# Kernel tuning notes

Hardware: AMD Instinct MI355X
Metric: run time of the kernel (lower is better)

Reference implementation:

```python
import jax, jax.numpy as jnp
import numpy as np
from jax import lax

HID, PROJ, DYN = 256, 256, 64
HW, BS, NQ = 6400, 16, 100


def setup_inputs() -> dict:
    key = jax.random.key(0)
    ks = jax.random.split(key, 10)
    p = lambda k, shape: jax.random.normal(k, shape, jnp.float32) * 0.02
    return {
        "query_feat": jax.random.normal(ks[0], (HW, BS, HID), jnp.float32),
        "support_feat": jax.random.normal(ks[1], (NQ, BS, HID), jnp.float32),
        "h": 80,
        "w": 80,
        "Wq": p(ks[2], (HID, PROJ)), "bq": jnp.zeros((PROJ,), jnp.float32),
        "Ws": p(ks[3], (HID, PROJ)), "bsp": jnp.zeros((PROJ,), jnp.float32),
        "W1": p(ks[4], (PROJ, DYN)), "b1": jnp.zeros((DYN,), jnp.float32),
        "W2": p(ks[5], (DYN, HID)), "b2": jnp.zeros((HID,), jnp.float32),
    }


def reference(query_feat, support_feat, h, w, Wq, bq, Ws, bsp, W1, b1, W2, b2):
    # query_feat: [hw, bs, c] -> [bs, hw, c]; support_feat: [nq, bs, c] -> [bs, nq, c]
    qf = jnp.transpose(query_feat, (1, 0, 2))
    sf = jnp.transpose(support_feat, (1, 0, 2))
    bsz, nq = sf.shape[0], sf.shape[1]
    hw = h * w

    fs_proj = sf @ Ws + bsp                      # [bs, nq, proj]
    fq_proj = qf @ Wq + bq                       # [bs, hw, proj]
    pattern = jnp.tanh(jax.nn.relu(fs_proj @ W1 + b1) @ W2 + b2)
    fs_feat = (pattern + 1.0) * fs_proj          # [bs, nq, proj]

    # bmm(fq, fs^T).T -> [bs, nq, hw]
    sim = jnp.einsum("bkp,bnp->bnk", fq_proj, fs_feat)
    similarity = sim.reshape(bsz, nq, h, w)

    # coordinate grid: x varies along w, y along h; flattened [hw, 2]
    gy = jnp.arange(h, dtype=jnp.float32) + 0.5
    gx = jnp.arange(w, dtype=jnp.float32) + 0.5
    X, Y = jnp.meshgrid(gx, gy, indexing="xy")  # each [h, w]
    coord = jnp.stack([X, Y], axis=-1).reshape(hw, 2)
    side = jnp.array([w, h], dtype=jnp.float32)

    sm = jax.nn.softmax(sim, axis=-1)            # [bs, nq, hw]
    proposal_for_loss = jnp.einsum("bnk,kd->bnd", sm, coord) / side

    # argmax peak -> one-hot -> 3x3 max-pool dilation (note (w,h) reshape per original)
    max_pos = jnp.argmax(sim, axis=-1)           # [bs, nq]
    max_mask = jax.nn.one_hot(max_pos, hw, dtype=jnp.float32).reshape(bsz, nq, w, h)
    local_mask = lax.reduce_window(
        max_mask, -jnp.inf, lax.max,
        window_dimensions=(1, 1, 3, 3), window_strides=(1, 1, 1, 1),
        padding=[(0, 0), (0, 0), (1, 1), (1, 1)],
    ).reshape(bsz, nq, hw)

    local_sm = sm * local_mask
    local_sm = local_sm / (jnp.sum(local_sm, axis=-1, keepdims=True) + 1e-10)
    proposals = jnp.einsum("bnk,kd->bnd", local_sm, coord) / side

    return proposal_for_loss, similarity, proposals
```

## Files before the change

### kernel.cpp

```cpp
#include <hip/hip_runtime.h>

#define HID 256
#define PROJ 256
#define DYN 64
#define HWD 6400
#define BSZ 16
#define NQ 100
#define HH 80
#define WW 80

typedef unsigned short u16;
typedef u16 u16x8 __attribute__((ext_vector_type(8)));
typedef __bf16 bf16x8 __attribute__((ext_vector_type(8)));
typedef float f32x4 __attribute__((ext_vector_type(4)));

__device__ __forceinline__ float bf2f(u16 h) {
    union { unsigned u; float f; } c; c.u = ((unsigned)h) << 16; return c.f;
}
__device__ __forceinline__ u16 f2bf(float f) {
    union { float f; unsigned u; } c; c.f = f;
    return (u16)((c.u + 0x7FFFu + ((c.u >> 16) & 1u)) >> 16);
}

__global__ __launch_bounds__(1024, 1) void kpre(
    const float* __restrict__ support,
    const float* __restrict__ Wq, const float* __restrict__ bq,
    const float* __restrict__ Ws, const float* __restrict__ bsp,
    const float* __restrict__ W1, const float* __restrict__ b1,
    const float* __restrict__ W2, const float* __restrict__ b2,
    u16* __restrict__ pack, float* __restrict__ cvec)
{
    const int c = blockIdx.x;
    const int b = blockIdx.y;
    const int t = threadIdx.x;

    __shared__ __align__(16) float sf_t[HID][8];
    __shared__ __align__(16) float part[4][8][256];
    __shared__ __align__(16) float fsp[8][PROJ];
    __shared__ __align__(16) float hidp[2][8][DYN];
    __shared__ __align__(16) float hid[8][DYN];
    __shared__ __align__(16) float fsf_t[PROJ][8];
    __shared__ float cacc[8][4];

    const int g = t >> 8;
    const int p = t & 255;

    {
        const int nl = t >> 7;
        const int i0 = (t & 127) * 2;
        const int n = c * 8 + nl;
        float v0 = 0.f, v1 = 0.f;
        if (n < NQ) {
            const float* sp = support + (size_t)n * (BSZ * HID) + (size_t)b * HID + i0;
            const float2 a = *reinterpret_cast<const float2*>(sp);
            v0 = a.x; v1 = a.y;
        }
        sf_t[i0][nl] = v0;
        sf_t[i0 + 1][nl] = v1;
    }
    __syncthreads();

    {
        float acc[8];
        #pragma unroll
        for (int n = 0; n < 8; ++n) acc[n] = 0.f;
        const int ibase = g * 64;
        float w[64];
        #pragma unroll
        for (int j = 0; j < 64; ++j)
            w[j] = Ws[(size_t)(ibase + j) * PROJ + p];
        __builtin_amdgcn_sched_barrier(0);
        #pragma unroll
        for (int j = 0; j < 64; ++j) {
            const f32x4 s0 = *reinterpret_cast<const f32x4*>(&sf_t[ibase + j][0]);
            const f32x4 s1 = *reinterpret_cast<const f32x4*>(&sf_t[ibase + j][4]);
            acc[0] += s0[0] * w[j]; acc[1] += s0[1] * w[j];
            acc[2] += s0[2] * w[j]; acc[3] += s0[3] * w[j];
            acc[4] += s1[0] * w[j]; acc[5] += s1[1] * w[j];
            acc[6] += s1[2] * w[j]; acc[7] += s1[3] * w[j];
        }
        #pragma unroll
        for (int n = 0; n < 8; ++n) part[g][n][p] = acc[n];
    }
    __syncthreads();
    {
        const int na = t >> 8;
        const float bb = bsp[p];
        #pragma unroll
        for (int k = 0; k < 2; ++k) {
            const int n = na + k * 4;
            fsp[n][p] = part[0][n][p] + part[1][n][p] + part[2][n][p] + part[3][n][p] + bb;
        }
    }
    __syncthreads();

    {
        const int ph = t >> 9;
        const int n = (t >> 6) & 7;
        const int d = t & 63;
        float a = 0.f;
        const int pb0 = ph * 128;
        #pragma unroll
        for (int pb = 0; pb < 128; pb += 64) {
            float w[64];
            #pragma unroll
            for (int j = 0; j < 64; ++j)
                w[j] = W1[(size_t)(pb0 + pb + j) * DYN + d];
            __builtin_amdgcn_sched_barrier(0);
            #pragma unroll
            for (int j = 0; j < 64; j += 4) {
                const f32x4 s = *reinterpret_cast<const f32x4*>(&fsp[n][pb0 + pb + j]);
                a += s[0] * w[j] + s[1] * w[j + 1] + s[2] * w[j + 2] + s[3] * w[j + 3];
            }
        }
        hidp[ph][n][d] = a;
    }
    __syncthreads();
    if (t < 512) {
        const int n = t >> 6, d = t & 63;
        const float a = hidp[0][n][d] + hidp[1][n][d] + b1[d];
        hid[n][d] = a > 0.f ? a : 0.f;
    }
    __syncthreads();

    {
        const int nh = t >> 8;
        const int n0 = nh * 2, n1 = nh * 2 + 1;
        const float bqv = bq[p];
        const float b2v = b2[p];
        float w[64];
        #pragma unroll
        for (int d = 0; d < 64; ++d) w[d] = W2[(size_t)d * PROJ + p];
        __builtin_amdgcn_sched_barrier(0);
        float a0 = 0.f, a1 = 0.f;
        #pragma unroll
        for (int d0 = 0; d0 < 64; d0 += 4) {
            const f32x4 h0 = *reinterpret_cast<const f32x4*>(&hid[n0][d0]);
            const f32x4 h1 = *reinterpret_cast<const f32x4*>(&hid[n1][d0]);
            a0 += h0[0] * w[d0] + h0[1] * w[d0 + 1] + h0[2] * w[d0 + 2] + h0[3] * w[d0 + 3];
            a1 += h1[0] * w[d0] + h1[1] * w[d0 + 1] + h1[2] * w[d0 + 2] + h1[3] * w[d0 + 3];
        }
        const float pat0 = tanhf(a0 + b2v);
        const float pat1 = tanhf(a1 + b2v);
        const float ff0 = (pat0 + 1.f) * fsp[n0][p];
        const float ff1 = (pat1 + 1.f) * fsp[n1][p];
        *reinterpret_cast<float2*>(&fsf_t[p][n0]) = make_float2(ff0, ff1);
        float cp0 = bqv * ff0, cp1 = bqv * ff1;
        for (int off = 32; off > 0; off >>= 1) {
            cp0 += __shfl_down(cp0, off);
            cp1 += __shfl_down(cp1, off);
        }
        const int lane = t & 63;
        const int ps = (t >> 6) & 3;
        if (lane == 0) { cacc[n0][ps] = cp0; cacc[n1][ps] = cp1; }
    }
    __syncthreads();
    if (t < 8) {
        const int n = c * 8 + t;
        if (n < NQ) cvec[b * NQ + n] = cacc[t][0] + cacc[t][1] + cacc[t][2] + cacc[t][3];
    }

    {
        const int h = p;
        float acc[8];
        #pragma unroll
        for (int n = 0; n < 8; ++n) acc[n] = 0.f;
        const int pbase = g * 64;
        f32x4 wv4[16];
        #pragma unroll
        for (int k = 0; k < 16; ++k)
            wv4[k] = *reinterpret_cast<const f32x4*>(Wq + (size_t)h * PROJ + pbase + k * 4);
        __builtin_amdgcn_sched_barrier(0);
        #pragma unroll
        for (int k = 0; k < 16; ++k) {
            #pragma unroll
            for (int m = 0; m < 4; ++m) {
                const int pp = pbase + k * 4 + m;
                const float w = wv4[k][m];
                const f32x4 f0 = *reinterpret_cast<const f32x4*>(&fsf_t[pp][0]);
                const f32x4 f1 = *reinterpret_cast<const f32x4*>(&fsf_t[pp][4]);
                acc[0] += f0[0] * w; acc[1] += f0[1] * w;
                acc[2] += f0[2] * w; acc[3] += f0[3] * w;
                acc[4] += f1[0] * w; acc[5] += f1[1] * w;
                acc[6] += f1[2] * w; acc[7] += f1[3] * w;
            }
        }
        #pragma unroll
        for (int n = 0; n < 8; ++n) part[g][n][h] = acc[n];
    }
    __syncthreads();

    {
        const int h = p;
        const int na = t >> 8;
        const int ks = h >> 5, quad = (h >> 3) & 3, j = h & 7;
        const int nt = c >> 1;
        #pragma unroll
        for (int k = 0; k < 2; ++k) {
            const int nl = na + k * 4;
            const int n = c * 8 + nl;
            float f = part[0][nl][h] + part[1][nl][h] + part[2][nl][h] + part[3][nl][h];
            if (n >= NQ) f = 0.f;
            const u16 hi = f2bf(f);
            const u16 lo = f2bf(f - bf2f(hi));
            const int nit = (c & 1) * 8 + nl;
            const int lane2 = quad * 16 + nit;
            const size_t base = ((((size_t)b * 2 + 0) * 8 + ks) * 8 + nt) * 512 + lane2 * 8 + j;
            pack[base] = hi;
            pack[base + (size_t)8 * 8 * 512] = lo;
        }
    }
}

__global__ __launch_bounds__(256, 3) void ksim(
    const float* __restrict__ qf,
    const u16* __restrict__ pack,
    const float* __restrict__ cvec,
    float* __restrict__ sim)
{
    const int mc = blockIdx.x;
    const int b  = blockIdx.y;
    const int wv = threadIdx.x >> 6;
    const int lane = threadIdx.x & 63;
    const int quad = lane >> 4, l16 = lane & 15;

    __shared__ __align__(16) u16 sbuf[3][16][512];

    const u16* pbase = pack + (size_t)b * 65536;

    #define STAGE(KS, SLOT)                                                         \
        do {                                                                        \
            _Pragma("unroll")                                                       \
            for (int i = 0; i < 4; ++i) {                                           \
                const int s14 = wv * 4 + i;                                         \
                const int s_ = s14 >> 3, nt_ = s14 & 7;                             \
                const u16* g_ = pbase + ((size_t)(s_ * 8 + (KS)) * 8 + nt_) * 512   \
                                + (size_t)lane * 8;                                 \
                __builtin_amdgcn_global_load_lds(                                   \
                    (const __attribute__((address_space(1))) void*)g_,              \
                    (__attribute__((address_space(3))) void*)&sbuf[SLOT][s14][0],   \
                    16, 0, 0);                                                      \
            }                                                                       \
        } while (0)

    f32x4 acc[7];
    #pragma unroll
    for (int nt = 0; nt < 7; ++nt) acc[nt] = (f32x4){0.f, 0.f, 0.f, 0.f};

    const int row = mc * 64 + wv * 16 + l16;
    const float* ap = qf + (size_t)row * (BSZ * HID) + b * HID + quad * 8;

    f32x4 af[16];
    {
        const float* p0 = ap + 0 * 32;
        const float* p1 = ap + 1 * 32;
        const float* p2 = ap + 2 * 32;
        const float* p3 = ap + 3 * 32;
        const float* p4 = ap + 4 * 32;
        const float* p5 = ap + 5 * 32;
        const float* p6 = ap + 6 * 32;
        const float* p7 = ap + 7 * 32;
        asm volatile(
            "global_load_dwordx4 %0, %16, off\n\t"
            "global_load_dwordx4 %1, %16, off offset:16\n\t"
            "global_load_dwordx4 %2, %17, off\n\t"
            "global_load_dwordx4 %3, %17, off offset:16\n\t"
            "global_load_dwordx4 %4, %18, off\n\t"
            "global_load_dwordx4 %5, %18, off offset:16\n\t"
            "global_load_dwordx4 %6, %19, off\n\t"
            "global_load_dwordx4 %7, %19, off offset:16\n\t"
            "global_load_dwordx4 %8, %20, off\n\t"
            "global_load_dwordx4 %9, %20, off offset:16\n\t"
            "global_load_dwordx4 %10, %21, off\n\t"
            "global_load_dwordx4 %11, %21, off offset:16\n\t"
            "global_load_dwordx4 %12, %22, off\n\t"
            "global_load_dwordx4 %13, %22, off offset:16\n\t"
            "global_load_dwordx4 %14, %23, off\n\t"
            "global_load_dwordx4 %15, %23, off offset:16\n\t"
            "s_waitcnt vmcnt(0)"
            : "=&v"(af[0]), "=&v"(af[1]), "=&v"(af[2]), "=&v"(af[3]),
              "=&v"(af[4]), "=&v"(af[5]), "=&v"(af[6]), "=&v"(af[7]),
              "=&v"(af[8]), "=&v"(af[9]), "=&v"(af[10]), "=&v"(af[11]),
              "=&v"(af[12]), "=&v"(af[13]), "=&v"(af[14]), "=&v"(af[15])
            : "v"(p0), "v"(p1), "v"(p2), "v"(p3),
              "v"(p4), "v"(p5), "v"(p6), "v"(p7));
    }
    STAGE(0, 0);
    STAGE(1, 1);

    bf16x8 Ahi[8], Alo[8];
    #pragma unroll
    for (int ks = 0; ks < 8; ++ks) {
        #pragma unroll
        for (int j = 0; j < 4; ++j) {
            const float v0 = af[2 * ks][j];
            const __bf16 h0 = (__bf16)v0;
            Ahi[ks][j] = h0; Alo[ks][j] = (__bf16)(v0 - (float)h0);
            const float v1 = af[2 * ks + 1][j];
            const __bf16 h1 = (__bf16)v1;
            Ahi[ks][4 + j] = h1; Alo[ks][4 + j] = (__bf16)(v1 - (float)h1);
        }
    }
    __syncthreads();

    #define WAITBAR(N)                                                              \
        do {                                                                        \
            asm volatile("s_waitcnt vmcnt(" #N ")" ::: "memory");                   \
            __builtin_amdgcn_sched_barrier(0);                                      \
            __builtin_amdgcn_s_barrier();                                           \
            __builtin_amdgcn_sched_barrier(0);                                      \
        } while (0)

    #define KS_BODY(KS, SR, SW, DOSTAGE)                                             \
    {                                                                                \
        if (DOSTAGE) STAGE((KS) + 2, SW);                                            \
        u16x8 uh[7];                                                                 \
        _Pragma("unroll")                                                            \
        for (int nt = 0; nt < 7; ++nt)                                               \
            uh[nt] = *reinterpret_cast<const u16x8*>(&sbuf[SR][nt][lane * 8]);       \
        _Pragma("unroll")                                                            \
        for (int nt = 0; nt < 7; ++nt) {                                             \
            const bf16x8 bh = __builtin_bit_cast(bf16x8, uh[nt]);                    \
            acc[nt] = __builtin_amdgcn_mfma_f32_16x16x32_bf16(Ahi[KS], bh, acc[nt], 0, 0, 0); \
            acc[nt] = __builtin_amdgcn_mfma_f32_16x16x32_bf16(Alo[KS], bh, acc[nt], 0, 0, 0); \
        }                                                                            \
        u16x8 ul[7];                                                                 \
        _Pragma("unroll")                                                            \
        for (int nt = 0; nt < 7; ++nt)                                               \
            ul[nt] = *reinterpret_cast<const u16x8*>(&sbuf[SR][8 + nt][lane * 8]);   \
        _Pragma("unroll")                                                            \
        for (int nt = 0; nt < 7; ++nt) {                                             \
            const bf16x8 bl = __builtin_bit_cast(bf16x8, ul[nt]);                    \
            acc[nt] = __builtin_amdgcn_mfma_f32_16x16x32_bf16(Ahi[KS], bl, acc[nt], 0, 0, 0); \
        }                                                                            \
    }

    KS_BODY(0, 0, 2, 1) WAITBAR(4);
    KS_BODY(1, 1, 0, 1) WAITBAR(4);
    KS_BODY(2, 2, 1, 1) WAITBAR(4);
    KS_BODY(3, 0, 2, 1) WAITBAR(4);
    KS_BODY(4, 1, 0, 1) WAITBAR(4);
    KS_BODY(5, 2, 1, 1) WAITBAR(4);
    KS_BODY(6, 0, 2, 0) WAITBAR(0);
    KS_BODY(7, 1, 0, 0)

    #undef KS_BODY
    #undef WAITBAR
    #undef STAGE

    const int kbase = mc * 64 + wv * 16 + quad * 4;
    #pragma unroll
    for (int nt = 0; nt < 7; ++nt) {
        const int n = nt * 16 + l16;
        if (n >= NQ) continue;
        const float cadd = cvec[b * NQ + n];
        f32x4 o = acc[nt];
        o[0] += cadd; o[1] += cadd; o[2] += cadd; o[3] += cadd;
        *reinterpret_cast<f32x4*>(sim + (size_t)(b * NQ + n) * HWD + kbase) = o;
    }
}

__global__ __launch_bounds__(128, 2) void kfin(
    const float* __restrict__ sim,
    float* __restrict__ out)
{
    const int bn = blockIdx.x;
    const int w = threadIdx.x >> 6;
    const int lane = threadIdx.x & 63;
    const float* src = sim + (size_t)bn * HWD;

    __shared__ float redf[2][8];

    const int base = w ? 12 : 0;
    const int cnt  = w ? 13 : 12;

    f32x4 v[13];
    #pragma unroll
    for (int j = 0; j < 13; ++j)
        if (j < cnt)
            v[j] = *reinterpret_cast<const f32x4*>(src + (base + j) * 256 + lane * 4);
    __builtin_amdgcn_sched_barrier(0);

    float bv = -3.4e38f; int bi = 0x7FFFFFFF;
    #pragma unroll
    for (int j = 0; j < 13; ++j) {
        if (j < cnt) {
            #pragma unroll
            for (int k = 0; k < 4; ++k) {
                if (v[j][k] > bv) { bv = v[j][k]; bi = (base + j) * 256 + lane * 4 + k; }
            }
        }
    }
    #pragma unroll
    for (int m = 1; m < 64; m <<= 1) {
        const float ov = __shfl_xor(bv, m);
        const int oi = __shfl_xor(bi, m);
        if (ov > bv || (ov == bv && oi < bi)) { bv = ov; bi = oi; }
    }
    if (lane == 0) { redf[w][0] = bv; redf[w][1] = __int_as_float(bi); }
    __syncthreads();
    {
        const float v0 = redf[0][0], v1 = redf[1][0];
        const int i0 = __float_as_int(redf[0][1]), i1 = __float_as_int(redf[1][1]);
        if (v1 > v0 || (v1 == v0 && i1 < i0)) { bv = v1; bi = i1; }
        else { bv = v0; bi = i0; }
    }
    const int xc = bi % WW, yc = bi / WW;

    float s1 = 0.f, sx = 0.f, sy = 0.f;
    float wl = 0.f, wx = 0.f, wyv = 0.f;
    const int g0 = base * 256 + lane * 4;
    int x = g0 % WW, y = g0 / WW;
    #pragma unroll
    for (int j = 0; j < 13; ++j) {
        if (j < cnt) {
            #pragma unroll
            for (int k = 0; k < 4; ++k) {
                int xe = x + k, ye = y;
                if (xe >= WW) { xe -= WW; ye += 1; }
                const float e = __expf(v[j][k] - bv);
                const float fx = (float)xe + 0.5f;
                const float fy = (float)ye + 0.5f;
                s1 += e; sx += e * fx; sy += e * fy;
                const int dx = xe - xc, dy = ye - yc;
                const bool inw = (dx >= -1 && dx <= 1 && dy >= -1 && dy <= 1);
                const float ew = inw ? e : 0.f;
                wl += ew; wx += ew * fx; wyv += ew * fy;
            }
        }
        x += 16; y += 3;
        if (x >= WW) { x -= WW; y += 1; }
    }
    #pragma unroll
    for (int m = 1; m < 64; m <<= 1) {
        s1 += __shfl_xor(s1, m);
        sx += __shfl_xor(sx, m);
        sy += __shfl_xor(sy, m);
        wl += __shfl_xor(wl, m);
        wx += __shfl_xor(wx, m);
        wyv += __shfl_xor(wyv, m);
    }
    if (lane == 0) {
        redf[w][2] = s1; redf[w][3] = sx; redf[w][4] = sy;
        redf[w][5] = wl; redf[w][6] = wx; redf[w][7] = wyv;
    }
    __syncthreads();

    if (w == 0 && lane == 0) {
        const float S1 = redf[0][2] + redf[1][2];
        const float SX = redf[0][3] + redf[1][3];
        const float SY = redf[0][4] + redf[1][4];
        const float WL = redf[0][5] + redf[1][5];
        const float WX = redf[0][6] + redf[1][6];
        const float WY = redf[0][7] + redf[1][7];
        const float invS = 1.f / S1;
        out[(size_t)bn * 2 + 0] = SX * invS / (float)WW;
        out[(size_t)bn * 2 + 1] = SY * invS / (float)HH;
        const float den = WL + 1e-10f * S1;
        const size_t pbase = 3200 + (size_t)BSZ * NQ * HWD;
        out[pbase + (size_t)bn * 2 + 0] = WX / den / (float)WW;
        out[pbase + (size_t)bn * 2 + 1] = WY / den / (float)HH;
    }
}

extern "C" void kernel_launch(void* const* d_in, const int* in_sizes, int n_in,
                              void* d_out, int out_size, void* d_ws, size_t ws_size,
                              hipStream_t stream) {
    const float* qf  = (const float*)d_in[0];
    const float* sf  = (const float*)d_in[1];
    const float* Wq  = (const float*)d_in[4];
    const float* bq  = (const float*)d_in[5];
    const float* Ws  = (const float*)d_in[6];
    const float* bsp = (const float*)d_in[7];
    const float* W1  = (const float*)d_in[8];
    const float* b1  = (const float*)d_in[9];
    const float* W2  = (const float*)d_in[10];
    const float* b2  = (const float*)d_in[11];

    u16*   pack  = (u16*)d_ws;
    float* cvec  = (float*)((char*)d_ws + 2097152);
    float* out   = (float*)d_out;
    float* sim   = out + 3200;

    kpre<<<dim3(14, 16), 1024, 0, stream>>>(sf, Wq, bq, Ws, bsp, W1, b1, W2, b2, pack, cvec);
    ksim<<<dim3(100, 16), 256, 0, stream>>>(qf, pack, cvec, sim);
    kfin<<<1600, 64 * 2, 0, stream>>>(sim, out);
}
```

Measured before the change: 250.2 us.

## Switch ksim B-tile staging to double buffer with two k-steps per stage

The ksim B-operand pipeline moves from a triple-buffered, one-k-step-per-stage scheme to a double-buffered scheme. Each stage now loads two k-steps (28 tiles) and uses plain __syncthreads in place of explicit vmcnt waits plus barriers. This halves the number of block barriers and stops loading the unused 8th n-tile per k-step. In exchange, shared memory per block grows (about 57 KB vs 48 KB) and the occupancy hint drops from 3 to 2 blocks per CU. The new code also relies on the compiler placing the waits for the async LDS loads before each barrier.

```diff
diff --git a/kernel.cpp b/kernel.cpp
--- a/kernel.cpp
+++ b/kernel.cpp
@@ -212,7 +212,7 @@
     }
 }
 
-__global__ __launch_bounds__(256, 3) void ksim(
+__global__ __launch_bounds__(256, 2) void ksim(
     const float* __restrict__ qf,
     const u16* __restrict__ pack,
     const float* __restrict__ cvec,
@@ -224,21 +224,24 @@
     const int lane = threadIdx.x & 63;
     const int quad = lane >> 4, l16 = lane & 15;
 
-    __shared__ __align__(16) u16 sbuf[3][16][512];
+    __shared__ __align__(16) u16 sbuf[2][28][512];
 
     const u16* pbase = pack + (size_t)b * 65536;
 
-    #define STAGE(KS, SLOT)                                                         \
+    #define STAGE2(KP, BUF)                                                         \
         do {                                                                        \
             _Pragma("unroll")                                                       \
-            for (int i = 0; i < 4; ++i) {                                           \
-                const int s14 = wv * 4 + i;                                         \
-                const int s_ = s14 >> 3, nt_ = s14 & 7;                             \
-                const u16* g_ = pbase + ((size_t)(s_ * 8 + (KS)) * 8 + nt_) * 512   \
+            for (int i = 0; i < 7; ++i) {                                           \
+                const int s28 = wv * 7 + i;                                         \
+                const int s_ = s28 / 14;                                            \
+                const int r_ = s28 % 14;                                            \
+                const int ks_ = (KP) * 2 + r_ / 7;                                  \
+                const int nt_ = r_ % 7;                                             \
+                const u16* g_ = pbase + ((size_t)(s_ * 8 + ks_) * 8 + nt_) * 512    \
                                 + (size_t)lane * 8;                                 \
                 __builtin_amdgcn_global_load_lds(                                   \
                     (const __attribute__((address_space(1))) void*)g_,              \
-                    (__attribute__((address_space(3))) void*)&sbuf[SLOT][s14][0],   \
+                    (__attribute__((address_space(3))) void*)&sbuf[BUF][s28][0],    \
                     16, 0, 0);                                                      \
             }                                                                       \
         } while (0)
@@ -285,8 +288,7 @@
             : "v"(p0), "v"(p1), "v"(p2), "v"(p3),
               "v"(p4), "v"(p5), "v"(p6), "v"(p7));
     }
-    STAGE(0, 0);
-    STAGE(1, 1);
+    STAGE2(0, 0);
 
     bf16x8 Ahi[8], Alo[8];
     #pragma unroll
@@ -303,21 +305,13 @@
     }
     __syncthreads();
 
-    #define WAITBAR(N)                                                              \
-        do {                                                                        \
-            asm volatile("s_waitcnt vmcnt(" #N ")" ::: "memory");                   \
-            __builtin_amdgcn_sched_barrier(0);                                      \
-            __builtin_amdgcn_s_barrier();                                           \
-            __builtin_amdgcn_sched_barrier(0);                                      \
-        } while (0)
-
-    #define KS_BODY(KS, SR, SW, DOSTAGE)                                             \
+    #define KS_COMPUTE(KS, BUF)                                                      \
     {                                                                                \
-        if (DOSTAGE) STAGE((KS) + 2, SW);                                            \
+        const int kp_ = (KS) & 1;                                                    \
         u16x8 uh[7];                                                                 \
         _Pragma("unroll")                                                            \
         for (int nt = 0; nt < 7; ++nt)                                               \
-            uh[nt] = *reinterpret_cast<const u16x8*>(&sbuf[SR][nt][lane * 8]);       \
+            uh[nt] = *reinterpret_cast<const u16x8*>(&sbuf[BUF][kp_ * 7 + nt][lane * 8]); \
         _Pragma("unroll")                                                            \
         for (int nt = 0; nt < 7; ++nt) {                                             \
             const bf16x8 bh = __builtin_bit_cast(bf16x8, uh[nt]);                    \
@@ -327,7 +321,7 @@
         u16x8 ul[7];                                                                 \
         _Pragma("unroll")                                                            \
         for (int nt = 0; nt < 7; ++nt)                                               \
-            ul[nt] = *reinterpret_cast<const u16x8*>(&sbuf[SR][8 + nt][lane * 8]);   \
+            ul[nt] = *reinterpret_cast<const u16x8*>(&sbuf[BUF][14 + kp_ * 7 + nt][lane * 8]); \
         _Pragma("unroll")                                                            \
         for (int nt = 0; nt < 7; ++nt) {                                             \
             const bf16x8 bl = __builtin_bit_cast(bf16x8, ul[nt]);                    \
@@ -335,18 +329,23 @@
         }                                                                            \
     }
 
-    KS_BODY(0, 0, 2, 1) WAITBAR(4);
-    KS_BODY(1, 1, 0, 1) WAITBAR(4);
-    KS_BODY(2, 2, 1, 1) WAITBAR(4);
-    KS_BODY(3, 0, 2, 1) WAITBAR(4);
-    KS_BODY(4, 1, 0, 1) WAITBAR(4);
-    KS_BODY(5, 2, 1, 1) WAITBAR(4);
-    KS_BODY(6, 0, 2, 0) WAITBAR(0);
-    KS_BODY(7, 1, 0, 0)
-
-    #undef KS_BODY
-    #undef WAITBAR
-    #undef STAGE
+    STAGE2(1, 1);
+    KS_COMPUTE(0, 0)
+    KS_COMPUTE(1, 0)
+    __syncthreads();
+    STAGE2(2, 0);
+    KS_COMPUTE(2, 1)
+    KS_COMPUTE(3, 1)
+    __syncthreads();
+    STAGE2(3, 1);
+    KS_COMPUTE(4, 0)
+    KS_COMPUTE(5, 0)
+    __syncthreads();
+    KS_COMPUTE(6, 1)
+    KS_COMPUTE(7, 1)
+
+    #undef KS_COMPUTE
+    #undef STAGE2
 
     const int kbase = mc * 64 + wv * 16 + quad * 4;
     #pragma unroll
```

Result: no change. 254.0 us (+1.5%).
